# Optimization experiments

Measured on AMD Instinct MI355X. Metric: run time of the kernel, lower is better.

The kernel has to match this reference:

```python
import jax, jax.numpy as jnp
import numpy as np

B, L, D, H, FF = 2, 2048, 1024, 16, 4096
DH = D // H
EPS = 1e-5  # torch LayerNorm default


def _layernorm(x, g, b):
    mu = jnp.mean(x, axis=-1, keepdims=True)
    var = jnp.mean(jnp.square(x - mu), axis=-1, keepdims=True)
    return (x - mu) * jax.lax.rsqrt(var + EPS) * g + b


def setup_inputs() -> dict:
    key = jax.random.key(0)
    ks = jax.random.split(key, 8)
    s = 0.02  # typical init scale for weights
    return {
        "x": jax.random.normal(ks[0], (B, L, D), jnp.float32),
        "pos_embed": jax.random.normal(ks[1], (1, L, D), jnp.float32) * s,
        "ln1_g": jnp.ones((D,), jnp.float32),
        "ln1_b": jnp.zeros((D,), jnp.float32),
        "Wq": jax.random.normal(ks[2], (D, D), jnp.float32) * s,
        "Wk": jax.random.normal(ks[3], (D, D), jnp.float32) * s,
        "Wv": jax.random.normal(ks[4], (D, D), jnp.float32) * s,
        "Wo": jax.random.normal(ks[5], (D, D), jnp.float32) * s,
        "bo": jnp.zeros((D,), jnp.float32),
        "ln2_g": jnp.ones((D,), jnp.float32),
        "ln2_b": jnp.zeros((D,), jnp.float32),
        "W1": jax.random.normal(ks[6], (D, FF), jnp.float32) * s,
        "b1": jnp.zeros((FF,), jnp.float32),
        "W2": jax.random.normal(ks[7], (FF, D), jnp.float32) * s,
        "b2": jnp.zeros((D,), jnp.float32),
    }


def reference(x, pos_embed, ln1_g, ln1_b, Wq, Wk, Wv, Wo, bo, ln2_g, ln2_b, W1, b1, W2, b2):
    scale = DH ** -0.5
    residual = x
    h = _layernorm(x, ln1_g, ln1_b) + pos_embed  # [B,L,D]
    # qkv projections (no bias, qkv_bias=False default), split into heads
    q = (h @ Wq).reshape(B, L, H, DH).transpose(0, 2, 1, 3)  # [B,H,L,DH]
    k = (h @ Wk).reshape(B, L, H, DH).transpose(0, 2, 1, 3)
    v = (h @ Wv).reshape(B, L, H, DH).transpose(0, 2, 1, 3)
    attn = jnp.einsum("bhqd,bhkd->bhqk", q, k) * scale  # [B,H,L,L]
    attn = jax.nn.softmax(attn, axis=-1)
    out = jnp.einsum("bhqk,bhkd->bhqd", attn, v)  # [B,H,L,DH]
    out = out.transpose(0, 2, 1, 3).reshape(B, L, D)
    out = out @ Wo + bo
    x = residual + out
    # MLP with pre-norm
    m = _layernorm(x, ln2_g, ln2_b)
    m = jax.nn.gelu(m @ W1 + b1, approximate=False) @ W2 + b2
    return x + m
```

## Files before the change

kernel.cpp:

```cpp
#include <hip/hip_runtime.h>
#include <hip/hip_bf16.h>
#include <cstdint>

typedef __bf16 bf16_t;
typedef __bf16 bf16x8 __attribute__((ext_vector_type(8)));
typedef __bf16 bf16x4v __attribute__((ext_vector_type(4)));
typedef short s16x4 __attribute__((ext_vector_type(4)));
typedef float f32x4 __attribute__((ext_vector_type(4)));

#define B_ 2
#define L_ 2048
#define D_ 1024
#define H_ 16
#define DH_ 64
#define FF_ 4096
#define M_TOT (B_*L_)

#define CLOG2 0.18033688011112042f


__device__ __forceinline__ void gload_lds16(const void* g, void* l) {
    __builtin_amdgcn_global_load_lds((__attribute__((address_space(1))) void*)g,
                                     (__attribute__((address_space(3))) void*)l,
                                     16, 0, 0);
}

__device__ __forceinline__ float fast_exp2(float v) {
    return __builtin_amdgcn_exp2f(v);
}

__device__ __forceinline__ float gelu_fast(float x) {
    float x3 = x * x * x;
    float y  = fmaf(0.044715f, x3, x);
    float e  = fast_exp2(y * 2.3022213f);
    float t  = fmaf(-2.0f, __builtin_amdgcn_rcpf(e + 1.0f), 1.0f);
    return 0.5f * x * (1.0f + t);
}

__global__ void transpose_bf16_kernel(const float* __restrict__ W, bf16_t* __restrict__ WT,
                                      int K, int N) {
    __shared__ float t[64][65];
    int tx = threadIdx.x, ty = threadIdx.y;
    int n0 = blockIdx.x * 64, k0 = blockIdx.y * 64;
#pragma unroll
    for (int i = 0; i < 4; i++) {
        int r = ty * 4 + i;
        float4 v = *(const float4*)(W + (size_t)(k0 + r) * N + n0 + tx * 4);
        t[r][tx * 4 + 0] = v.x; t[r][tx * 4 + 1] = v.y;
        t[r][tx * 4 + 2] = v.z; t[r][tx * 4 + 3] = v.w;
    }
    __syncthreads();
#pragma unroll
    for (int i = 0; i < 4; i++) {
        int r = ty * 4 + i;
        bf16x4v pk;
#pragma unroll
        for (int j = 0; j < 4; j++) pk[j] = (bf16_t)t[tx * 4 + j][r];
        *(bf16x4v*)(WT + (size_t)(n0 + r) * K + k0 + tx * 4) = pk;
    }
}

__global__ void transpose_qkvo_kernel(const float* __restrict__ Wq, const float* __restrict__ Wk,
                                      const float* __restrict__ Wv, const float* __restrict__ Wo,
                                      bf16_t* __restrict__ WqkvT, bf16_t* __restrict__ WoT) {
    int z = blockIdx.z;
    const float* W = (z == 0) ? Wq : (z == 1) ? Wk : (z == 2) ? Wv : Wo;
    bf16_t* dst = (z < 3) ? (WqkvT + (size_t)z * 1024 * 1024) : WoT;
    __shared__ float t[64][65];
    int tx = threadIdx.x, ty = threadIdx.y;
    int n0 = blockIdx.x * 64, k0 = blockIdx.y * 64;
#pragma unroll
    for (int i = 0; i < 4; i++) {
        int r = ty * 4 + i;
        float4 v = *(const float4*)(W + (size_t)(k0 + r) * D_ + n0 + tx * 4);
        t[r][tx * 4 + 0] = v.x; t[r][tx * 4 + 1] = v.y;
        t[r][tx * 4 + 2] = v.z; t[r][tx * 4 + 3] = v.w;
    }
    __syncthreads();
#pragma unroll
    for (int i = 0; i < 4; i++) {
        int r = ty * 4 + i;
        bf16x4v pk;
#pragma unroll
        for (int j = 0; j < 4; j++) pk[j] = (bf16_t)t[tx * 4 + j][r];
        *(bf16x4v*)(dst + (size_t)(n0 + r) * D_ + k0 + tx * 4) = pk;
    }
}

__global__ __launch_bounds__(256) void ln_kernel(const float* __restrict__ x,
                                                 const float* __restrict__ pos,
                                                 const float* __restrict__ g,
                                                 const float* __restrict__ beta,
                                                 bf16_t* __restrict__ out) {
    int row = blockIdx.x, tid = threadIdx.x;
    const float* xr = x + (size_t)row * D_;
    float v[4];
    float s = 0.f, sq = 0.f;
#pragma unroll
    for (int i = 0; i < 4; i++) {
        float a = xr[tid + 256 * i];
        v[i] = a; s += a; sq += a * a;
    }
#pragma unroll
    for (int o = 32; o > 0; o >>= 1) { s += __shfl_xor(s, o); sq += __shfl_xor(sq, o); }
    __shared__ float red[8];
    int wid = tid >> 6;
    if ((tid & 63) == 0) { red[wid] = s; red[4 + wid] = sq; }
    __syncthreads();
    s  = red[0] + red[1] + red[2] + red[3];
    sq = red[4] + red[5] + red[6] + red[7];
    float mu  = s * (1.f / D_);
    float var = sq * (1.f / D_) - mu * mu;
    float rs  = rsqrtf(var + 1e-5f);
    int l = row & (L_ - 1);
#pragma unroll
    for (int i = 0; i < 4; i++) {
        int c = tid + 256 * i;
        float hv = (v[i] - mu) * rs * g[c] + beta[c];
        if (pos) hv += pos[(size_t)l * D_ + c];
        out[(size_t)row * D_ + c] = (bf16_t)hv;
    }
}

__global__ __launch_bounds__(256) void ln_fuse_kernel(const float* __restrict__ x,
                                                      const float* __restrict__ bo,
                                                      const float* __restrict__ P0,
                                                      const float* __restrict__ P1,
                                                      const float* __restrict__ g,
                                                      const float* __restrict__ beta,
                                                      float* __restrict__ x2,
                                                      bf16_t* __restrict__ out) {
    int row = blockIdx.x, tid = threadIdx.x;
    size_t base = (size_t)row * D_;
    float v[4];
    float s = 0.f, sq = 0.f;
#pragma unroll
    for (int i = 0; i < 4; i++) {
        int c = tid + 256 * i;
        float a = x[base + c] + bo[c] + P0[base + c] + P1[base + c];
        v[i] = a; s += a; sq += a * a;
        x2[base + c] = a;
    }
#pragma unroll
    for (int o = 32; o > 0; o >>= 1) { s += __shfl_xor(s, o); sq += __shfl_xor(sq, o); }
    __shared__ float red[8];
    int wid = tid >> 6;
    if ((tid & 63) == 0) { red[wid] = s; red[4 + wid] = sq; }
    __syncthreads();
    s  = red[0] + red[1] + red[2] + red[3];
    sq = red[4] + red[5] + red[6] + red[7];
    float mu  = s * (1.f / D_);
    float var = sq * (1.f / D_) - mu * mu;
    float rs  = rsqrtf(var + 1e-5f);
#pragma unroll
    for (int i = 0; i < 4; i++) {
        int c = tid + 256 * i;
        out[base + c] = (bf16_t)((v[i] - mu) * rs * g[c] + beta[c]);
    }
}

__global__ __launch_bounds__(256) void reduce_out_kernel(const float* __restrict__ x2,
                                                         const float* __restrict__ bias,
                                                         const float* __restrict__ P1,
                                                         float* __restrict__ dout) {
    int i = (blockIdx.x * 256 + threadIdx.x) * 4;
    float4 a  = *(const float4*)(x2 + i);
    float4 bv = *(const float4*)(bias + (i & (D_ - 1)));
    float4 p0 = *(const float4*)(dout + i);
    float4 p1 = *(const float4*)(P1 + i);
    a.x += bv.x + p0.x + p1.x;
    a.y += bv.y + p0.y + p1.y;
    a.z += bv.z + p0.z + p1.z;
    a.w += bv.w + p0.w + p1.w;
    *(float4*)(dout + i) = a;
}

template <int EPI, typename OutT>
__global__ __launch_bounds__(256) void gemm_kernel(const bf16_t* __restrict__ A,
                                                   const bf16_t* __restrict__ BT,
                                                   OutT* __restrict__ C,
                                                   const float* __restrict__ bias,
                                                   bf16_t* __restrict__ Vt,
                                                   int M, int N, int K) {
    __shared__ __align__(16) bf16_t sA[2][128 * 32];
    __shared__ __align__(16) bf16_t sB[2][128 * 32];
    int tid = threadIdx.x;
    int lane = tid & 63, w = tid >> 6, wy = w >> 1, wx = w & 1;
    int qm = lane & 15, quad = lane >> 4;
    int row0 = blockIdx.x * 128, col0 = blockIdx.y * 128;
    f32x4 acc[4][4] = {};
    int sf[2], sra[2], scol[2];
#pragma unroll
    for (int c = 0; c < 2; c++) {
        int f = tid * 8 + c * 2048;
        sf[c] = f;
        sra[c] = f >> 5;
        int ch = (f >> 3) & 3;
        scol[c] = ((ch ^ ((sra[c] >> 1) & 3)) << 3);
    }
    int aoff[4], boff[4];
#pragma unroll
    for (int t = 0; t < 4; t++) {
        int Ra = wy * 64 + t * 16 + qm;
        int Rb = wx * 64 + t * 16 + qm;
        aoff[t] = Ra * 32 + ((quad ^ ((Ra >> 1) & 3)) << 3);
        boff[t] = Rb * 32 + ((quad ^ ((Rb >> 1) & 3)) << 3);
    }
    const bf16_t* Ab = A  + (size_t)row0 * K;
    const bf16_t* Bb = BT + (size_t)col0 * K;
#pragma unroll
    for (int c = 0; c < 2; c++) {
        gload_lds16(Ab + (size_t)sra[c] * K + scol[c], &sA[0][sf[c]]);
        gload_lds16(Bb + (size_t)sra[c] * K + scol[c], &sB[0][sf[c]]);
    }
    for (int k0 = 0; k0 < K; k0 += 32) {
        int cur = (k0 >> 5) & 1;
        __syncthreads();
        int kn = k0 + 32;
        if (kn < K) {
#pragma unroll
            for (int c = 0; c < 2; c++) {
                gload_lds16(Ab + (size_t)sra[c] * K + kn + scol[c], &sA[cur ^ 1][sf[c]]);
                gload_lds16(Bb + (size_t)sra[c] * K + kn + scol[c], &sB[cur ^ 1][sf[c]]);
            }
        }
        bf16x8 af[4], bfr[4];
#pragma unroll
        for (int mt = 0; mt < 4; mt++) af[mt] = *(const bf16x8*)&sA[cur][aoff[mt]];
#pragma unroll
        for (int nt = 0; nt < 4; nt++) bfr[nt] = *(const bf16x8*)&sB[cur][boff[nt]];
#pragma unroll
        for (int mt = 0; mt < 4; mt++)
#pragma unroll
            for (int nt = 0; nt < 4; nt++)
                acc[mt][nt] = __builtin_amdgcn_mfma_f32_16x16x32_bf16(af[mt], bfr[nt],
                                                                      acc[mt][nt], 0, 0, 0);
    }
    if (EPI == 4 && col0 >= 2048) {
#pragma unroll
        for (int mt = 0; mt < 4; mt++) {
            int row_base = row0 + wy * 64 + mt * 16 + quad * 4;
            int bb = row_base >> 11, key0 = row_base & 2047;
#pragma unroll
            for (int nt = 0; nt < 4; nt++) {
                int vcol = col0 - 2048 + wx * 64 + nt * 16 + qm;
                int hh = vcol >> 6, dd = vcol & 63;
                bf16x4v pk;
#pragma unroll
                for (int r = 0; r < 4; r++) pk[r] = (bf16_t)acc[mt][nt][r];
                *(bf16x4v*)&Vt[(size_t)(((bb << 4) + hh) * 64 + dd) * 2048 + key0] = pk;
            }
        }
        return;
    }
    float qscale = (EPI == 4 && col0 < 1024) ? CLOG2 : 1.0f;
#pragma unroll
    for (int mt = 0; mt < 4; mt++) {
#pragma unroll
        for (int nt = 0; nt < 4; nt++) {
            int col = col0 + wx * 64 + nt * 16 + qm;
#pragma unroll
            for (int r = 0; r < 4; r++) {
                int row = row0 + wy * 64 + mt * 16 + quad * 4 + r;
                float v = acc[mt][nt][r];
                if (EPI == 2) { v += bias[col]; v = gelu_fast(v); }
                if (EPI == 4) C[(size_t)row * 2048 + col] = (OutT)(v * qscale);
                else          C[(size_t)row * N + col] = (OutT)v;
            }
        }
    }
}

__global__ __launch_bounds__(512, 2) void gemm256_gelu_kernel(const bf16_t* __restrict__ A,
                                                              const bf16_t* __restrict__ BT,
                                                              bf16_t* __restrict__ C,
                                                              const float* __restrict__ bias,
                                                              int N, int K) {
    __shared__ __align__(16) bf16_t sA[2][256 * 32];
    __shared__ __align__(16) bf16_t sB[2][256 * 32];
    int tid = threadIdx.x;
    int lane = tid & 63, w = tid >> 6, wy = w >> 2, wx = w & 3;
    int qm = lane & 15, quad = lane >> 4;
    int row0 = blockIdx.x * 256, col0 = blockIdx.y * 256;
    f32x4 acc[8][4] = {};
    int sf[2], sra[2], scol[2];
#pragma unroll
    for (int c = 0; c < 2; c++) {
        int f = tid * 8 + c * 4096;
        sf[c] = f;
        sra[c] = f >> 5;
        int ch = (f >> 3) & 3;
        scol[c] = ((ch ^ ((sra[c] >> 1) & 3)) << 3);
    }
    int aoff[8], boff[4];
#pragma unroll
    for (int t = 0; t < 8; t++) {
        int Ra = wy * 128 + t * 16 + qm;
        aoff[t] = Ra * 32 + ((quad ^ ((Ra >> 1) & 3)) << 3);
    }
#pragma unroll
    for (int t = 0; t < 4; t++) {
        int Rb = wx * 64 + t * 16 + qm;
        boff[t] = Rb * 32 + ((quad ^ ((Rb >> 1) & 3)) << 3);
    }
    const bf16_t* Ab = A  + (size_t)row0 * K;
    const bf16_t* Bb = BT + (size_t)col0 * K;
#pragma unroll
    for (int c = 0; c < 2; c++) {
        gload_lds16(Ab + (size_t)sra[c] * K + scol[c], &sA[0][sf[c]]);
        gload_lds16(Bb + (size_t)sra[c] * K + scol[c], &sB[0][sf[c]]);
    }
    for (int k0 = 0; k0 < K; k0 += 32) {
        int cur = (k0 >> 5) & 1;
        __syncthreads();
        int kn = k0 + 32;
        if (kn < K) {
#pragma unroll
            for (int c = 0; c < 2; c++) {
                gload_lds16(Ab + (size_t)sra[c] * K + kn + scol[c], &sA[cur ^ 1][sf[c]]);
                gload_lds16(Bb + (size_t)sra[c] * K + kn + scol[c], &sB[cur ^ 1][sf[c]]);
            }
        }
        bf16x8 bfr[4];
#pragma unroll
        for (int nt = 0; nt < 4; nt++) bfr[nt] = *(const bf16x8*)&sB[cur][boff[nt]];
#pragma unroll
        for (int mt = 0; mt < 8; mt++) {
            bf16x8 af = *(const bf16x8*)&sA[cur][aoff[mt]];
#pragma unroll
            for (int nt = 0; nt < 4; nt++)
                acc[mt][nt] = __builtin_amdgcn_mfma_f32_16x16x32_bf16(af, bfr[nt],
                                                                      acc[mt][nt], 0, 0, 0);
        }
    }
#pragma unroll
    for (int mt = 0; mt < 8; mt++) {
#pragma unroll
        for (int nt = 0; nt < 4; nt++) {
            int col = col0 + wx * 64 + nt * 16 + qm;
            float bv = bias[col];
#pragma unroll
            for (int r = 0; r < 4; r++) {
                int row = row0 + wy * 128 + mt * 16 + quad * 4 + r;
                C[(size_t)row * N + col] = (bf16_t)gelu_fast(acc[mt][nt][r] + bv);
            }
        }
    }
}

__global__ __launch_bounds__(256) void gemm_splitk_st_kernel(const bf16_t* __restrict__ A,
                                                             const bf16_t* __restrict__ BT,
                                                             float* __restrict__ P0,
                                                             float* __restrict__ P1,
                                                             int N, int Ktot, int Ksplit) {
    __shared__ __align__(16) bf16_t sA[2][128 * 32];
    __shared__ __align__(16) bf16_t sB[2][128 * 32];
    int tid = threadIdx.x;
    int lane = tid & 63, w = tid >> 6, wy = w >> 1, wx = w & 1;
    int qm = lane & 15, quad = lane >> 4;
    int row0 = blockIdx.x * 128, col0 = blockIdx.y * 128;
    size_t koff = (size_t)blockIdx.z * Ksplit;
    f32x4 acc[4][4] = {};
    int sf[2], sra[2], scol[2];
#pragma unroll
    for (int c = 0; c < 2; c++) {
        int f = tid * 8 + c * 2048;
        sf[c] = f;
        sra[c] = f >> 5;
        int ch = (f >> 3) & 3;
        scol[c] = ((ch ^ ((sra[c] >> 1) & 3)) << 3);
    }
    int aoff[4], boff[4];
#pragma unroll
    for (int t = 0; t < 4; t++) {
        int Ra = wy * 64 + t * 16 + qm;
        int Rb = wx * 64 + t * 16 + qm;
        aoff[t] = Ra * 32 + ((quad ^ ((Ra >> 1) & 3)) << 3);
        boff[t] = Rb * 32 + ((quad ^ ((Rb >> 1) & 3)) << 3);
    }
    const bf16_t* Ab = A  + (size_t)row0 * Ktot + koff;
    const bf16_t* Bb = BT + (size_t)col0 * Ktot + koff;
#pragma unroll
    for (int c = 0; c < 2; c++) {
        gload_lds16(Ab + (size_t)sra[c] * Ktot + scol[c], &sA[0][sf[c]]);
        gload_lds16(Bb + (size_t)sra[c] * Ktot + scol[c], &sB[0][sf[c]]);
    }
    for (int k0 = 0; k0 < Ksplit; k0 += 32) {
        int cur = (k0 >> 5) & 1;
        __syncthreads();
        int kn = k0 + 32;
        if (kn < Ksplit) {
#pragma unroll
            for (int c = 0; c < 2; c++) {
                gload_lds16(Ab + (size_t)sra[c] * Ktot + kn + scol[c], &sA[cur ^ 1][sf[c]]);
                gload_lds16(Bb + (size_t)sra[c] * Ktot + kn + scol[c], &sB[cur ^ 1][sf[c]]);
            }
        }
        bf16x8 af[4], bfr[4];
#pragma unroll
        for (int mt = 0; mt < 4; mt++) af[mt] = *(const bf16x8*)&sA[cur][aoff[mt]];
#pragma unroll
        for (int nt = 0; nt < 4; nt++) bfr[nt] = *(const bf16x8*)&sB[cur][boff[nt]];
#pragma unroll
        for (int mt = 0; mt < 4; mt++)
#pragma unroll
            for (int nt = 0; nt < 4; nt++)
                acc[mt][nt] = __builtin_amdgcn_mfma_f32_16x16x32_bf16(af[mt], bfr[nt],
                                                                      acc[mt][nt], 0, 0, 0);
    }
    float* P = blockIdx.z ? P1 : P0;
#pragma unroll
    for (int mt = 0; mt < 4; mt++) {
#pragma unroll
        for (int nt = 0; nt < 4; nt++) {
            int col = col0 + wx * 64 + nt * 16 + qm;
#pragma unroll
            for (int r = 0; r < 4; r++) {
                int row = row0 + wy * 64 + mt * 16 + quad * 4 + r;
                P[(size_t)row * N + col] = acc[mt][nt][r];
            }
        }
    }
}

__global__ __launch_bounds__(256) void attn_kernel(const bf16_t* __restrict__ QK,
                                                   const bf16_t* __restrict__ Vt,
                                                   bf16_t* __restrict__ O) {
    __shared__ __align__(16) bf16_t sK[2][64 * 64];
    __shared__ __align__(16) bf16_t sV[2][64 * 64];
    int tid = threadIdx.x, lane = tid & 63, w = tid >> 6;
    int qm = lane & 15, quad = lane >> 4;
    int q0 = blockIdx.x * 128 + w * 32;
    int bh = blockIdx.y, b = bh >> 4, h = bh & 15;

    const bf16_t* Qbase = QK + (size_t)(b * L_) * 2048 + h * 64;
    const bf16_t* Kbase = Qbase + 1024;
    const bf16_t* Vbase = Vt + (size_t)bh * 64 * 2048;

    bf16x8 qf[2][2];
#pragma unroll
    for (int g = 0; g < 2; g++) {
        const bf16_t* qp = Qbase + (size_t)(q0 + g * 16 + qm) * 2048 + quad * 8;
        qf[g][0] = *(const bf16x8*)qp;
        qf[g][1] = *(const bf16x8*)(qp + 32);
    }

    int f0 = tid * 8, f1 = f0 + 2048;
    int r0 = f0 >> 6, sc0 = ((((f0 >> 3) & 7) ^ (r0 & 7)) << 3);
    int r1 = f1 >> 6, sc1 = ((((f1 >> 3) & 7) ^ (r1 & 7)) << 3);

    gload_lds16(Kbase + (size_t)r0 * 2048 + sc0, &sK[0][f0]);
    gload_lds16(Kbase + (size_t)r1 * 2048 + sc1, &sK[0][f1]);
    gload_lds16(Vbase + (size_t)r0 * 2048 + sc0, &sV[0][f0]);
    gload_lds16(Vbase + (size_t)r1 * 2048 + sc1, &sV[0][f1]);

    f32x4 o[2][4] = {};
    float l_[2] = {0.f, 0.f};

    int kfo[4][2], vfo[4][4];
#pragma unroll
    for (int kt = 0; kt < 4; kt++) {
#pragma unroll
        for (int ks = 0; ks < 2; ks++) {
            int row = kt * 16 + qm;
            kfo[kt][ks] = row * 64 + ((((ks << 2) + quad) ^ (row & 7)) << 3);
        }
#pragma unroll
        for (int dt = 0; dt < 4; dt++) {
            int row = dt * 16 + qm;
            int cw = (kt << 1) + (quad >> 1);
            vfo[dt][kt] = row * 64 + ((cw ^ (row & 7)) << 3) + ((quad & 1) << 2);
        }
    }

    for (int kv0 = 0; kv0 < L_; kv0 += 64) {
        int cur = (kv0 >> 6) & 1;
        __syncthreads();
        int kn = kv0 + 64;
        if (kn < L_) {
            gload_lds16(Kbase + (size_t)(kn + r0) * 2048 + sc0, &sK[cur ^ 1][f0]);
            gload_lds16(Kbase + (size_t)(kn + r1) * 2048 + sc1, &sK[cur ^ 1][f1]);
            gload_lds16(Vbase + (size_t)r0 * 2048 + kn + sc0, &sV[cur ^ 1][f0]);
            gload_lds16(Vbase + (size_t)r1 * 2048 + kn + sc1, &sV[cur ^ 1][f1]);
        }

        bf16x8 kf[4][2];
#pragma unroll
        for (int kt = 0; kt < 4; kt++)
#pragma unroll
            for (int ks = 0; ks < 2; ks++)
                kf[kt][ks] = *(const bf16x8*)&sK[cur][kfo[kt][ks]];
        f32x4 s[2][4] = {};
        __builtin_amdgcn_s_setprio(1);
#pragma unroll
        for (int kt = 0; kt < 4; kt++)
#pragma unroll
            for (int ks = 0; ks < 2; ks++) {
                s[0][kt] = __builtin_amdgcn_mfma_f32_16x16x32_bf16(kf[kt][ks], qf[0][ks], s[0][kt], 0, 0, 0);
                s[1][kt] = __builtin_amdgcn_mfma_f32_16x16x32_bf16(kf[kt][ks], qf[1][ks], s[1][kt], 0, 0, 0);
            }
        __builtin_amdgcn_s_setprio(0);

        s16x4 pf[2][4];
#pragma unroll
        for (int g = 0; g < 2; g++) {
            float sum = l_[g];
#pragma unroll
            for (int kt = 0; kt < 4; kt++) {
                union { bf16x4v b; s16x4 i; } u;
#pragma unroll
                for (int r = 0; r < 4; r++) {
                    float p = fast_exp2(s[g][kt][r]);
                    sum += p;
                    u.b[r] = (bf16_t)p;
                }
                pf[g][kt] = u.i;
            }
            l_[g] = sum;
        }

        __builtin_amdgcn_s_setprio(1);
#pragma unroll
        for (int dt = 0; dt < 4; dt++)
#pragma unroll
            for (int kt = 0; kt < 4; kt++) {
                s16x4 vf = *(const s16x4*)&sV[cur][vfo[dt][kt]];
                o[0][dt] = __builtin_amdgcn_mfma_f32_16x16x16bf16_1k(vf, pf[0][kt], o[0][dt], 0, 0, 0);
                o[1][dt] = __builtin_amdgcn_mfma_f32_16x16x16bf16_1k(vf, pf[1][kt], o[1][dt], 0, 0, 0);
            }
        __builtin_amdgcn_s_setprio(0);
    }

#pragma unroll
    for (int g = 0; g < 2; g++) {
        float lt = l_[g];
        lt += __shfl_xor(lt, 16);
        lt += __shfl_xor(lt, 32);
        float rl = 1.0f / lt;
        size_t row = (size_t)(b * L_ + q0 + g * 16 + qm);
#pragma unroll
        for (int dt = 0; dt < 4; dt++) {
            bf16x4v pk;
#pragma unroll
            for (int r = 0; r < 4; r++) pk[r] = (bf16_t)(o[g][dt][r] * rl);
            *(bf16x4v*)&O[row * D_ + h * 64 + dt * 16 + quad * 4] = pk;
        }
    }
}


extern "C" void kernel_launch(void* const* d_in, const int* in_sizes, int n_in,
                              void* d_out, int out_size, void* d_ws, size_t ws_size,
                              hipStream_t stream) {
    const float* x   = (const float*)d_in[0];
    const float* pos = (const float*)d_in[1];
    const float* g1  = (const float*)d_in[2];
    const float* be1 = (const float*)d_in[3];
    const float* Wq  = (const float*)d_in[4];
    const float* Wk  = (const float*)d_in[5];
    const float* Wv  = (const float*)d_in[6];
    const float* Wo  = (const float*)d_in[7];
    const float* bo  = (const float*)d_in[8];
    const float* g2  = (const float*)d_in[9];
    const float* be2 = (const float*)d_in[10];
    const float* W1  = (const float*)d_in[11];
    const float* b1m = (const float*)d_in[12];
    const float* W2  = (const float*)d_in[13];
    const float* b2m = (const float*)d_in[14];

    char* ws = (char*)d_ws;
    const size_t MB = 1ull << 20;
    bf16_t* W2T   = (bf16_t*)(ws + 0);
    float*  x2    = (float*) (ws + 8 * MB);
    bf16_t* qk    = (bf16_t*)(ws + 24 * MB);
    bf16_t* Vt    = (bf16_t*)(ws + 40 * MB);
    bf16_t* hb    = (bf16_t*)(ws + 48 * MB);
    float*  Pwo0  = (float*) (ws + 24 * MB);
    float*  Pwo1  = (float*) (ws + 40 * MB);
    bf16_t* attnO = (bf16_t*)(ws + 56 * MB);
    bf16_t* mb    = (bf16_t*)(ws + 56 * MB);
    bf16_t* ff1   = (bf16_t*)(ws + 24 * MB);
    bf16_t* W1T   = (bf16_t*)(ws + 64 * MB);
    float*  Pff1  = (float*) (ws + 56 * MB);
    bf16_t* WqkvT = (bf16_t*)(ws + 72 * MB);
    bf16_t* WoT   = (bf16_t*)(ws + 78 * MB);

    dim3 tt(16, 16);
    transpose_qkvo_kernel<<<dim3(16, 16, 4), tt, 0, stream>>>(Wq, Wk, Wv, Wo, WqkvT, WoT);
    transpose_bf16_kernel<<<dim3(64, 16), tt, 0, stream>>>(W1, W1T, D_, FF_);
    transpose_bf16_kernel<<<dim3(16, 64), tt, 0, stream>>>(W2, W2T, FF_, D_);

    ln_kernel<<<M_TOT, 256, 0, stream>>>(x, pos, g1, be1, hb);

    gemm_kernel<4, bf16_t><<<dim3(32, 24), 256, 0, stream>>>(hb, WqkvT, qk, nullptr,
                                                             Vt, M_TOT, 3072, D_);

    attn_kernel<<<dim3(16, 32), 256, 0, stream>>>(qk, Vt, attnO);

    gemm_splitk_st_kernel<<<dim3(32, 8, 2), 256, 0, stream>>>(attnO, WoT, Pwo0, Pwo1,
                                                              D_, D_, D_ / 2);

    ln_fuse_kernel<<<M_TOT, 256, 0, stream>>>(x, bo, Pwo0, Pwo1, g2, be2, x2, mb);

    gemm256_gelu_kernel<<<dim3(16, 16), 512, 0, stream>>>(mb, W1T, ff1, b1m, FF_, D_);

    gemm_splitk_st_kernel<<<dim3(32, 8, 2), 256, 0, stream>>>(ff1, W2T, (float*)d_out,
                                                              Pff1, D_, FF_, FF_ / 2);

    reduce_out_kernel<<<M_TOT * D_ / 1024, 256, 0, stream>>>(x2, b2m, Pff1, (float*)d_out);

    (void)in_sizes; (void)n_in; (void)out_size; (void)ws_size;
}
```

Before: 365.3 us.

## Load K/V fragments directly from global memory in attention, dropping LDS staging

```diff
diff --git a/kernel.cpp b/kernel.cpp
--- a/kernel.cpp
+++ b/kernel.cpp
@@ -426,15 +426,13 @@
 __global__ __launch_bounds__(256) void attn_kernel(const bf16_t* __restrict__ QK,
                                                    const bf16_t* __restrict__ Vt,
                                                    bf16_t* __restrict__ O) {
-    __shared__ __align__(16) bf16_t sK[2][64 * 64];
-    __shared__ __align__(16) bf16_t sV[2][64 * 64];
     int tid = threadIdx.x, lane = tid & 63, w = tid >> 6;
     int qm = lane & 15, quad = lane >> 4;
     int q0 = blockIdx.x * 128 + w * 32;
     int bh = blockIdx.y, b = bh >> 4, h = bh & 15;
 
     const bf16_t* Qbase = QK + (size_t)(b * L_) * 2048 + h * 64;
-    const bf16_t* Kbase = Qbase + 1024;
+    const bf16_t* Kbase = QK + (size_t)(b * L_) * 2048 + h * 64 + 1024;
     const bf16_t* Vbase = Vt + (size_t)bh * 64 * 2048;
 
     bf16x8 qf[2][2];
@@ -445,51 +443,27 @@
         qf[g][1] = *(const bf16x8*)(qp + 32);
     }
 
-    int f0 = tid * 8, f1 = f0 + 2048;
-    int r0 = f0 >> 6, sc0 = ((((f0 >> 3) & 7) ^ (r0 & 7)) << 3);
-    int r1 = f1 >> 6, sc1 = ((((f1 >> 3) & 7) ^ (r1 & 7)) << 3);
-
-    gload_lds16(Kbase + (size_t)r0 * 2048 + sc0, &sK[0][f0]);
-    gload_lds16(Kbase + (size_t)r1 * 2048 + sc1, &sK[0][f1]);
-    gload_lds16(Vbase + (size_t)r0 * 2048 + sc0, &sV[0][f0]);
-    gload_lds16(Vbase + (size_t)r1 * 2048 + sc1, &sV[0][f1]);
+    const bf16_t* Kl = Kbase + (size_t)qm * 2048 + quad * 8;
+    const bf16_t* Vl = Vbase + (size_t)qm * 2048 + quad * 4;
 
     f32x4 o[2][4] = {};
     float l_[2] = {0.f, 0.f};
 
-    int kfo[4][2], vfo[4][4];
-#pragma unroll
-    for (int kt = 0; kt < 4; kt++) {
-#pragma unroll
-        for (int ks = 0; ks < 2; ks++) {
-            int row = kt * 16 + qm;
-            kfo[kt][ks] = row * 64 + ((((ks << 2) + quad) ^ (row & 7)) << 3);
-        }
-#pragma unroll
-        for (int dt = 0; dt < 4; dt++) {
-            int row = dt * 16 + qm;
-            int cw = (kt << 1) + (quad >> 1);
-            vfo[dt][kt] = row * 64 + ((cw ^ (row & 7)) << 3) + ((quad & 1) << 2);
-        }
-    }
-
     for (int kv0 = 0; kv0 < L_; kv0 += 64) {
-        int cur = (kv0 >> 6) & 1;
-        __syncthreads();
-        int kn = kv0 + 64;
-        if (kn < L_) {
-            gload_lds16(Kbase + (size_t)(kn + r0) * 2048 + sc0, &sK[cur ^ 1][f0]);
-            gload_lds16(Kbase + (size_t)(kn + r1) * 2048 + sc1, &sK[cur ^ 1][f1]);
-            gload_lds16(Vbase + (size_t)r0 * 2048 + kn + sc0, &sV[cur ^ 1][f0]);
-            gload_lds16(Vbase + (size_t)r1 * 2048 + kn + sc1, &sV[cur ^ 1][f1]);
-        }
+        s16x4 vf[4][4];
+#pragma unroll
+        for (int dt = 0; dt < 4; dt++)
+#pragma unroll
+            for (int kt = 0; kt < 4; kt++)
+                vf[dt][kt] = *(const s16x4*)(Vl + (size_t)(dt * 16) * 2048 + kv0 + kt * 16);
 
         bf16x8 kf[4][2];
 #pragma unroll
         for (int kt = 0; kt < 4; kt++)
 #pragma unroll
             for (int ks = 0; ks < 2; ks++)
-                kf[kt][ks] = *(const bf16x8*)&sK[cur][kfo[kt][ks]];
+                kf[kt][ks] = *(const bf16x8*)(Kl + (size_t)(kv0 + kt * 16) * 2048 + ks * 32);
+
         f32x4 s[2][4] = {};
         __builtin_amdgcn_s_setprio(1);
 #pragma unroll
@@ -507,12 +481,12 @@
             float sum = l_[g];
 #pragma unroll
             for (int kt = 0; kt < 4; kt++) {
-                union { bf16x4v b; s16x4 i; } u;
+                union { bf16x4v bv; s16x4 i; } u;
 #pragma unroll
                 for (int r = 0; r < 4; r++) {
                     float p = fast_exp2(s[g][kt][r]);
                     sum += p;
-                    u.b[r] = (bf16_t)p;
+                    u.bv[r] = (bf16_t)p;
                 }
                 pf[g][kt] = u.i;
             }
@@ -524,9 +498,8 @@
         for (int dt = 0; dt < 4; dt++)
 #pragma unroll
             for (int kt = 0; kt < 4; kt++) {
-                s16x4 vf = *(const s16x4*)&sV[cur][vfo[dt][kt]];
-                o[0][dt] = __builtin_amdgcn_mfma_f32_16x16x16bf16_1k(vf, pf[0][kt], o[0][dt], 0, 0, 0);
-                o[1][dt] = __builtin_amdgcn_mfma_f32_16x16x16bf16_1k(vf, pf[1][kt], o[1][dt], 0, 0, 0);
+                o[0][dt] = __builtin_amdgcn_mfma_f32_16x16x16bf16_1k(vf[dt][kt], pf[0][kt], o[0][dt], 0, 0, 0);
+                o[1][dt] = __builtin_amdgcn_mfma_f32_16x16x16bf16_1k(vf[dt][kt], pf[1][kt], o[1][dt], 0, 0, 0);
             }
         __builtin_amdgcn_s_setprio(0);
     }
```

New measurement: 482.4 us. 1.32x slower.
